# Optimization experiments

Hardware: AMD Instinct MI355X
Metric: run time of the kernel (lower is better)

## Reference

```python
import jax, jax.numpy as jnp
import numpy as np

# Config matching init_kwargs
TAUS = [0.25, 0.5, 0.75]
QWEIGHTS = [0.25, 0.5, 0.25]
T_THRESH = 10
K_DIL = 2
EPS_GIN = 0.0  # (1 + eps) * x term; train_eps=False


def setup_inputs() -> dict:
    key = jax.random.key(0)
    k0, k1, k2, k3 = jax.random.split(key, 4)
    B, N, C, H, CO = 4, 512, 64, 128, 64
    x = jax.random.normal(k0, (B, N, C), dtype=jnp.float32)
    # symmetric random binary adjacency, ~30 avg degree -> dilation active (m > T)
    u = jax.random.uniform(k1, (B, N, N))
    a = (u < 0.03).astype(jnp.float32)
    adj = jnp.maximum(a, jnp.swapaxes(a, 1, 2))
    # last 32 nodes are padding
    mask = jnp.broadcast_to(jnp.arange(N) < (N - 32), (B, N))
    W1 = jax.random.normal(k2, (C, H), dtype=jnp.float32) * (1.0 / np.sqrt(C))
    b1 = jnp.zeros((H,), dtype=jnp.float32)
    W2 = jax.random.normal(k3, (H, CO), dtype=jnp.float32) * (1.0 / np.sqrt(H))
    b2 = jnp.zeros((CO,), dtype=jnp.float32)
    return {"x": x, "adj": adj, "mask": mask, "W1": W1, "b1": b1, "W2": W2, "b2": b2}


def _dilate_adj(adj, mask):
    """Vectorized form of the per-node Python-loop dilation.
    Decisions are based on adj_ (with self-loops), exactly as in the torch loop."""
    B, N, _ = adj.shape
    eye = jnp.eye(N, dtype=bool)
    adj_ = jnp.where(eye[None], 1.0, adj)                 # add self-loops
    nb = (adj_ > 0) & (~eye)[None]                         # neighbors w/o self (B,N,N)
    m = nb.sum(-1)                                         # neighbor count (B,N)
    rank = jnp.cumsum(nb, axis=-1) - 1                     # 0-based position among neighbors
    skip = jnp.where(m > T_THRESH, (m + K_DIL - 1) // K_DIL, 1)  # ceil(m/k); linear mode, layer_idx=1
    do_dil = (skip > 1) & mask                             # masked-out rows are skipped
    removed = nb & do_dil[..., None] & (((rank + 1) % skip[..., None]) == 0)
    rem = removed | jnp.swapaxes(removed, 1, 2)            # symmetric removal
    return jnp.where(rem, 0.0, adj_)


def _weighted_nanquantile_agg(x, valid):
    """Weighted sum of linear-interpolated quantiles over the ragged neighbor dim.
    x: (B,N,C), valid: (B,N,N) bool -> (B,N,C). Empty rows -> 0 (nan_to_num)."""
    B, N, C = x.shape
    big = jnp.finfo(x.dtype).max / 4
    # pool of neighbor features, invalid slots pushed to the end of the sort
    vals = jnp.where(valid[..., None], x[:, None, :, :], big)   # (B,N,N,C)
    sv = jnp.sort(vals, axis=2)
    m = valid.sum(-1)                                           # (B,N)
    mf = m.astype(x.dtype)

    def gather(idx):  # idx (B,N) int -> (B,N,C)
        idxb = jnp.broadcast_to(idx[:, :, None, None], (B, N, 1, C))
        return jnp.take_along_axis(sv, idxb, axis=2)[:, :, 0, :]

    agg = jnp.zeros_like(x)
    for tau, wt in zip(TAUS, QWEIGHTS):
        pos = jnp.clip(tau * (mf - 1.0), 0.0)                   # torch 'linear' interpolation
        lo = jnp.floor(pos).astype(jnp.int32)
        hi = jnp.ceil(pos).astype(jnp.int32)
        frac = (pos - lo.astype(x.dtype))[..., None]
        q = gather(lo) * (1.0 - frac) + gather(hi) * frac
        agg = agg + wt * q
    return jnp.where((m > 0)[..., None], agg, 0.0)


def reference(x, adj, mask, W1, b1, W2, b2):
    dtp = x.dtype
    adj_d = _dilate_adj(adj, mask)
    agg = _weighted_nanquantile_agg(x, adj_d > 0)
    out = (1.0 + EPS_GIN) * x + agg
    h = jax.nn.relu(jnp.einsum('bnc,ch->bnh', out, W1) + b1)    # GIN MLP
    y = jnp.einsum('bnh,ho->bno', h, W2) + b2
    return y * mask[..., None].astype(dtp)
```

## Files before the change

### kernel.cpp

```cpp
#include <hip/hip_runtime.h>
#include <stdint.h>

#define NB 4
#define NN 512
#define NC 64
#define NH 128
#define NCO 64
#define MAXM 64
#define SST 65
#define FBIG 3.0e38f

__device__ inline bool read_mask(const void* mp, int idx) {
    const int* ip = (const int*)mp;
    int w0 = ip[0];
    if (w0 == 1) return ip[idx] != 0;
    if (w0 == 0x3f800000) return ((const float*)mp)[idx] != 0.0f;
    return ((const unsigned char*)mp)[idx] != 0;
}

__global__ __launch_bounds__(256) void prep_kernel(
        const float* __restrict__ adj, const void* __restrict__ maskp,
        const float* __restrict__ W1, const float* __restrict__ W2,
        uint64_t* __restrict__ validbits, float* __restrict__ W1T,
        float* __restrict__ W2T, int dowt)
{
    int wave = (blockIdx.x * 256 + threadIdx.x) >> 6;
    int lane = threadIdx.x & 63;
    if (wave < NB * NN) {
        int i = wave & (NN - 1);
        const float* arow = adj + (size_t)wave * NN;
        uint64_t ball[8];
        int m = 0;
        #pragma unroll
        for (int k = 0; k < 8; ++k) {
            int j = k * 64 + lane;
            bool f = (j != i) && (arow[j] > 0.0f);
            uint64_t bl = __ballot(f);
            ball[k] = bl;
            m += __popcll(bl);
        }
        int skip = (m > 10) ? ((m + 1) >> 1) : 1;
        bool dodil = (skip > 1) && read_mask(maskp, wave);
        int skip2 = skip * 2;
        int prefix = 0;
        #pragma unroll
        for (int k = 0; k < 8; ++k) {
            uint64_t bl = ball[k];
            int rank1 = prefix + __popcll(bl & ((1ull << lane) - 1ull)) + 1;
            bool f = (bl >> lane) & 1ull;
            bool keep = f && !(dodil && (rank1 == skip || rank1 == skip2));
            uint64_t vb = __ballot(keep);
            if (lane == 0) validbits[(size_t)wave * 8 + k] = vb;
            prefix += __popcll(bl);
        }
    }
    if (dowt) {
        int e = blockIdx.x * 256 + threadIdx.x;
        if (e < 8192) {
            int k = e >> 6, c = e & 63;
            W1T[e] = W1[c * NH + k];
        } else if (e < 16384) {
            int e2 = e - 8192;
            int o = e2 >> 7, k = e2 & 127;
            W2T[e2] = W2[k * NCO + o];
        }
    }
}

template<int WIDTH>
__device__ inline float bitonic_sort_lane(float v, int lane) {
    #pragma unroll
    for (int k = 2; k <= WIDTH; k <<= 1) {
        #pragma unroll
        for (int d = k >> 1; d >= 1; d >>= 1) {
            float vp = __shfl_xor(v, d);
            bool keepmin = ((lane & k) == 0) == ((lane & d) == 0);
            v = keepmin ? fminf(v, vp) : fmaxf(v, vp);
        }
    }
    return v;
}

template<bool USE_WT>
__global__ void fused_kernel(
        const float* __restrict__ x,
        const void* __restrict__ maskp,
        const float* __restrict__ W1,
        const float* __restrict__ b1,
        const float* __restrict__ W2,
        const float* __restrict__ b2,
        const uint64_t* __restrict__ validbits,
        const float* __restrict__ W1T,
        const float* __restrict__ W2T,
        float* __restrict__ out)
{
    int row = blockIdx.x;
    int b = row >> 9, i = row & (NN - 1);
    int tid = threadIdx.x, lane = tid & 63, wv = tid >> 6;
    float* outp = out + (size_t)row * NCO;

    if (!read_mask(maskp, row)) {
        if (tid < NCO) outp[tid] = 0.0f;
        return;
    }

    __shared__ float sv[NC * SST];
    __shared__ float s_agg[NC];
    __shared__ __align__(8) uint16_t s_idx[MAXM];
    __shared__ uint64_t s_vb[8];
    __shared__ uint64_t s_vf[8];
    __shared__ int s_cnt;

    float xval = (tid < NC) ? x[(size_t)row * NC + tid] : 0.0f;
    if (tid < 8) s_vb[tid] = validbits[(size_t)row * 8 + tid];
    if (tid < MAXM) s_idx[tid] = (uint16_t)i;
    if (tid == 0) s_cnt = 1;
    __syncthreads();

    int ic = i >> 6;
    uint64_t imask = 1ull << (i & 63);
    #pragma unroll
    for (int it = 0; it < 2; ++it) {
        int j = tid + it * 256;
        bool nb = ((s_vb[j >> 6] >> (j & 63)) & 1ull) &&
                  (validbits[((size_t)(b * NN + j)) * 8 + ic] & imask);
        uint64_t bl = __ballot(nb || (j == i));
        if (lane == 0) s_vf[it * 4 + wv] = bl;
        if (nb) {
            int p = atomicAdd(&s_cnt, 1);
            if (p < MAXM) s_idx[p] = (uint16_t)j;
        }
    }
    __syncthreads();
    int m = s_cnt;

    float mf = (float)m;
    const float taus[3] = {0.25f, 0.5f, 0.75f};
    const float wts[3]  = {0.25f, 0.5f, 0.25f};
    int tlo[3], thi[3];
    float tfrac[3];
    #pragma unroll
    for (int t = 0; t < 3; ++t) {
        float pos = taus[t] * (mf - 1.0f);
        float fl = floorf(pos);
        tlo[t] = (int)fl;
        thi[t] = (int)ceilf(pos);
        tfrac[t] = pos - fl;
    }

    const float* xb = x + (size_t)b * NN * NC;

    if (m <= 32) {
        #pragma unroll
        for (int h = 0; h < 2; ++h) {
            ushort4 id4 = ((const ushort4*)s_idx)[wv * 2 + h];
            int j0 = wv * 8 + h * 4;
            float v0 = xb[(int)id4.x * NC + lane];
            float v1 = xb[(int)id4.y * NC + lane];
            float v2 = xb[(int)id4.z * NC + lane];
            float v3 = xb[(int)id4.w * NC + lane];
            sv[lane * SST + j0 + 0] = (j0 + 0 < m) ? v0 : FBIG;
            sv[lane * SST + j0 + 1] = (j0 + 1 < m) ? v1 : FBIG;
            sv[lane * SST + j0 + 2] = (j0 + 2 < m) ? v2 : FBIG;
            sv[lane * SST + j0 + 3] = (j0 + 3 < m) ? v3 : FBIG;
        }
        __syncthreads();
        int half = lane >> 5, l = lane & 31;
        #pragma unroll
        for (int pp = 0; pp < 8; ++pp) {
            int p = pp * 4 + wv;
            int c = p * 2 + half;
            float v = sv[c * SST + l];
            v = bitonic_sort_lane<32>(v, l);
            float agg = 0.0f;
            #pragma unroll
            for (int t = 0; t < 3; ++t) {
                float vlo = __shfl(v, (half << 5) | tlo[t]);
                float vhi = __shfl(v, (half << 5) | thi[t]);
                agg += wts[t] * (vlo * (1.0f - tfrac[t]) + vhi * tfrac[t]);
            }
            if (l == 0) s_agg[c] = agg;
        }
    } else if (m <= MAXM) {
        #pragma unroll
        for (int h = 0; h < 4; ++h) {
            ushort4 id4 = ((const ushort4*)s_idx)[wv * 4 + h];
            int j0 = wv * 16 + h * 4;
            float v0 = xb[(int)id4.x * NC + lane];
            float v1 = xb[(int)id4.y * NC + lane];
            float v2 = xb[(int)id4.z * NC + lane];
            float v3 = xb[(int)id4.w * NC + lane];
            sv[lane * SST + j0 + 0] = (j0 + 0 < m) ? v0 : FBIG;
            sv[lane * SST + j0 + 1] = (j0 + 1 < m) ? v1 : FBIG;
            sv[lane * SST + j0 + 2] = (j0 + 2 < m) ? v2 : FBIG;
            sv[lane * SST + j0 + 3] = (j0 + 3 < m) ? v3 : FBIG;
        }
        __syncthreads();
        #pragma unroll
        for (int cc = 0; cc < 16; ++cc) {
            int c = cc * 4 + wv;
            float v = sv[c * SST + lane];
            v = bitonic_sort_lane<64>(v, lane);
            float agg = 0.0f;
            #pragma unroll
            for (int t = 0; t < 3; ++t) {
                float vlo = __shfl(v, tlo[t]);
                float vhi = __shfl(v, thi[t]);
                agg += wts[t] * (vlo * (1.0f - tfrac[t]) + vhi * tfrac[t]);
            }
            if (lane == 0) s_agg[c] = agg;
        }
    } else {
        if (tid < NC) {
            int c = tid;
            float qv[6];
            for (int j1 = 0; j1 < NN; ++j1) {
                if (!((s_vf[j1 >> 6] >> (j1 & 63)) & 1ull)) continue;
                float v1 = xb[j1 * NC + c];
                int rs = 0, rl = 0;
                for (int j2 = 0; j2 < NN; ++j2) {
                    if (!((s_vf[j2 >> 6] >> (j2 & 63)) & 1ull)) continue;
                    float v2 = xb[j2 * NC + c];
                    rs += v2 < v1;
                    rl += v2 <= v1;
                }
                #pragma unroll
                for (int t = 0; t < 3; ++t) {
                    if (rs <= tlo[t] && tlo[t] < rl) qv[2 * t]     = v1;
                    if (rs <= thi[t] && thi[t] < rl) qv[2 * t + 1] = v1;
                }
            }
            float agg = 0.0f;
            #pragma unroll
            for (int t = 0; t < 3; ++t)
                agg += wts[t] * (qv[2 * t] * (1.0f - tfrac[t]) + qv[2 * t + 1] * tfrac[t]);
            s_agg[c] = agg;
        }
    }
    __syncthreads();

    float* s_out  = sv;
    float* s_h    = sv + 64;
    float* s_hp   = sv + 256;
    float* s_part = sv + 512;

    if (tid < NC)
        s_out[tid] = xval + s_agg[tid];
    __syncthreads();

    {
        int k = tid & 127, g = tid >> 7;
        float acc = 0.0f;
        if (USE_WT) {
            const float4* w = (const float4*)(W1T + k * 64 + g * 32);
            #pragma unroll
            for (int q = 0; q < 8; ++q) {
                float4 wq = w[q];
                int cc = g * 32 + q * 4;
                acc += wq.x * s_out[cc] + wq.y * s_out[cc + 1]
                     + wq.z * s_out[cc + 2] + wq.w * s_out[cc + 3];
            }
        } else {
            for (int cc = g * 32; cc < g * 32 + 32; ++cc)
                acc += s_out[cc] * W1[cc * NH + k];
        }
        s_hp[g * NH + k] = acc;
    }
    __syncthreads();
    if (tid < NH) {
        float a = s_hp[tid] + s_hp[NH + tid] + b1[tid];
        s_h[tid] = a > 0.0f ? a : 0.0f;
    }
    __syncthreads();

    {
        int o = tid & 63, g = tid >> 6;
        float acc = 0.0f;
        if (USE_WT) {
            const float4* w = (const float4*)(W2T + o * 128 + g * 32);
            #pragma unroll
            for (int q = 0; q < 8; ++q) {
                float4 wq = w[q];
                int k = g * 32 + q * 4;
                acc += wq.x * s_h[k] + wq.y * s_h[k + 1]
                     + wq.z * s_h[k + 2] + wq.w * s_h[k + 3];
            }
        } else {
            for (int k = g * 32; k < g * 32 + 32; ++k)
                acc += s_h[k] * W2[k * NCO + o];
        }
        s_part[g * NCO + o] = acc;
    }
    __syncthreads();
    if (tid < NCO)
        outp[tid] = s_part[tid] + s_part[64 + tid] + s_part[128 + tid]
                  + s_part[192 + tid] + b2[tid];
}

extern "C" void kernel_launch(void* const* d_in, const int* in_sizes, int n_in,
                              void* d_out, int out_size, void* d_ws, size_t ws_size,
                              hipStream_t stream) {
    const float* x   = (const float*)d_in[0];
    const float* adj = (const float*)d_in[1];
    const void* mask = d_in[2];
    const float* W1  = (const float*)d_in[3];
    const float* b1  = (const float*)d_in[4];
    const float* W2  = (const float*)d_in[5];
    const float* b2  = (const float*)d_in[6];
    float* out = (float*)d_out;

    uint64_t* validbits = (uint64_t*)d_ws;
    float* W1T = (float*)((char*)d_ws + 131072);
    float* W2T = W1T + 8192;
    int dowt = (ws_size >= 196608) ? 1 : 0;

    prep_kernel<<<512, 256, 0, stream>>>(adj, mask, W1, W2, validbits, W1T, W2T, dowt);
    if (dowt)
        fused_kernel<true><<<NB * NN, 256, 0, stream>>>(
            x, mask, W1, b1, W2, b2, validbits, W1T, W2T, out);
    else
        fused_kernel<false><<<NB * NN, 256, 0, stream>>>(
            x, mask, W1, b1, W2, b2, validbits, W1T, W2T, out);
}
```

Measured before the change: 115.5 us.

## Sort neighbor features in registers with 4-per-lane bitonic network, drop LDS staging

Replaces the LDS-staged transpose plus one-value-per-lane bitonic sort with a scheme where each lane loads four neighbor values for one channel directly from global memory and sorts them with a hybrid register/shuffle bitonic network. Several channels are handled per wave at once, and quantiles are read back through select plus shuffle. This removes the large shared buffer, a __syncthreads, and many cross-lane shuffle stages, which also shrinks LDS use and may raise occupancy. The cost is uncoalesced gather loads (lanes index different channels and rows) and a more intricate sort network.

```diff
diff --git a/kernel.cpp b/kernel.cpp
--- a/kernel.cpp
+++ b/kernel.cpp
@@ -7,7 +7,6 @@
 #define NH 128
 #define NCO 64
 #define MAXM 64
-#define SST 65
 #define FBIG 3.0e38f
 
 __device__ inline bool read_mask(const void* mp, int idx) {
@@ -67,17 +66,48 @@
     }
 }
 
-template<int WIDTH>
-__device__ inline float bitonic_sort_lane(float v, int lane) {
+__device__ inline void cmpsw(float& a, float& b, bool asc) {
+    float lo = fminf(a, b), hi = fmaxf(a, b);
+    a = asc ? lo : hi;
+    b = asc ? hi : lo;
+}
+__device__ inline void xstage(float q[4], int g, int ld, bool asc) {
     #pragma unroll
-    for (int k = 2; k <= WIDTH; k <<= 1) {
-        #pragma unroll
-        for (int d = k >> 1; d >= 1; d >>= 1) {
-            float vp = __shfl_xor(v, d);
-            bool keepmin = ((lane & k) == 0) == ((lane & d) == 0);
-            v = keepmin ? fminf(v, vp) : fmaxf(v, vp);
-        }
-    }
+    for (int r = 0; r < 4; ++r) {
+        float vp = __shfl_xor(q[r], ld);
+        bool mn = ((g & ld) == 0) == asc;
+        q[r] = mn ? fminf(q[r], vp) : fmaxf(q[r], vp);
+    }
+}
+__device__ inline void regstages(float q[4], bool a) {
+    cmpsw(q[0], q[2], a); cmpsw(q[1], q[3], a);
+    cmpsw(q[0], q[1], a); cmpsw(q[2], q[3], a);
+}
+__device__ inline void sort64_4(float q[4], int g) {
+    cmpsw(q[0], q[1], true);  cmpsw(q[2], q[3], false);
+    regstages(q, (g & 1) == 0);
+    { bool a = (g & 2) == 0; xstage(q, g, 1, a); regstages(q, a); }
+    { bool a = (g & 4) == 0; xstage(q, g, 2, a); xstage(q, g, 1, a);
+      regstages(q, a); }
+    { bool a = (g & 8) == 0; xstage(q, g, 4, a); xstage(q, g, 2, a);
+      xstage(q, g, 1, a); regstages(q, a); }
+    { xstage(q, g, 8, true); xstage(q, g, 4, true); xstage(q, g, 2, true);
+      xstage(q, g, 1, true); regstages(q, true); }
+}
+__device__ inline void sort32_4(float q[4], int g) {
+    cmpsw(q[0], q[1], true);  cmpsw(q[2], q[3], false);
+    regstages(q, (g & 1) == 0);
+    { bool a = (g & 2) == 0; xstage(q, g, 1, a); regstages(q, a); }
+    { bool a = (g & 4) == 0; xstage(q, g, 2, a); xstage(q, g, 1, a);
+      regstages(q, a); }
+    { xstage(q, g, 4, true); xstage(q, g, 2, true); xstage(q, g, 1, true);
+      regstages(q, true); }
+}
+__device__ inline float selreg(const float q[4], int r) {
+    float v = q[0];
+    v = (r == 1) ? q[1] : v;
+    v = (r == 2) ? q[2] : v;
+    v = (r == 3) ? q[3] : v;
     return v;
 }
 
@@ -104,11 +134,14 @@
         return;
     }
 
-    __shared__ float sv[NC * SST];
-    __shared__ float s_agg[NC];
     __shared__ __align__(8) uint16_t s_idx[MAXM];
     __shared__ uint64_t s_vb[8];
     __shared__ uint64_t s_vf[8];
+    __shared__ float s_agg[NC];
+    __shared__ float s_out[NC];
+    __shared__ float s_h[NH];
+    __shared__ float s_hp[2 * NH];
+    __shared__ float s_part[4 * NCO];
     __shared__ int s_cnt;
 
     float xval = (tid < NC) ? x[(size_t)row * NC + tid] : 0.0f;
@@ -151,64 +184,52 @@
     const float* xb = x + (size_t)b * NN * NC;
 
     if (m <= 32) {
+        int g = lane & 7, sg = lane >> 3;
+        ushort4 id4 = ((const ushort4*)s_idx)[g];
+        int j0 = g * 4;
         #pragma unroll
-        for (int h = 0; h < 2; ++h) {
-            ushort4 id4 = ((const ushort4*)s_idx)[wv * 2 + h];
-            int j0 = wv * 8 + h * 4;
-            float v0 = xb[(int)id4.x * NC + lane];
-            float v1 = xb[(int)id4.y * NC + lane];
-            float v2 = xb[(int)id4.z * NC + lane];
-            float v3 = xb[(int)id4.w * NC + lane];
-            sv[lane * SST + j0 + 0] = (j0 + 0 < m) ? v0 : FBIG;
-            sv[lane * SST + j0 + 1] = (j0 + 1 < m) ? v1 : FBIG;
-            sv[lane * SST + j0 + 2] = (j0 + 2 < m) ? v2 : FBIG;
-            sv[lane * SST + j0 + 3] = (j0 + 3 < m) ? v3 : FBIG;
-        }
-        __syncthreads();
-        int half = lane >> 5, l = lane & 31;
+        for (int p = 0; p < 2; ++p) {
+            int c = p * 32 + wv * 8 + sg;
+            float q[4];
+            q[0] = (j0 + 0 < m) ? xb[(int)id4.x * NC + c] : FBIG;
+            q[1] = (j0 + 1 < m) ? xb[(int)id4.y * NC + c] : FBIG;
+            q[2] = (j0 + 2 < m) ? xb[(int)id4.z * NC + c] : FBIG;
+            q[3] = (j0 + 3 < m) ? xb[(int)id4.w * NC + c] : FBIG;
+            sort32_4(q, g);
+            float agg = 0.0f;
+            #pragma unroll
+            for (int t = 0; t < 3; ++t) {
+                float sl = selreg(q, tlo[t] & 3);
+                float vlo = __shfl(sl, (lane & 56) | (tlo[t] >> 2));
+                float sh = selreg(q, thi[t] & 3);
+                float vhi = __shfl(sh, (lane & 56) | (thi[t] >> 2));
+                agg += wts[t] * (vlo * (1.0f - tfrac[t]) + vhi * tfrac[t]);
+            }
+            if (g == 0) s_agg[c] = agg;
+        }
+    } else if (m <= MAXM) {
+        int g = lane & 15, sg = lane >> 4;
+        ushort4 id4 = ((const ushort4*)s_idx)[g];
+        int j0 = g * 4;
         #pragma unroll
-        for (int pp = 0; pp < 8; ++pp) {
-            int p = pp * 4 + wv;
-            int c = p * 2 + half;
-            float v = sv[c * SST + l];
-            v = bitonic_sort_lane<32>(v, l);
+        for (int p = 0; p < 4; ++p) {
+            int c = p * 16 + wv * 4 + sg;
+            float q[4];
+            q[0] = (j0 + 0 < m) ? xb[(int)id4.x * NC + c] : FBIG;
+            q[1] = (j0 + 1 < m) ? xb[(int)id4.y * NC + c] : FBIG;
+            q[2] = (j0 + 2 < m) ? xb[(int)id4.z * NC + c] : FBIG;
+            q[3] = (j0 + 3 < m) ? xb[(int)id4.w * NC + c] : FBIG;
+            sort64_4(q, g);
             float agg = 0.0f;
             #pragma unroll
             for (int t = 0; t < 3; ++t) {
-                float vlo = __shfl(v, (half << 5) | tlo[t]);
-                float vhi = __shfl(v, (half << 5) | thi[t]);
+                float sl = selreg(q, tlo[t] & 3);
+                float vlo = __shfl(sl, (lane & 48) | (tlo[t] >> 2));
+                float sh = selreg(q, thi[t] & 3);
+                float vhi = __shfl(sh, (lane & 48) | (thi[t] >> 2));
                 agg += wts[t] * (vlo * (1.0f - tfrac[t]) + vhi * tfrac[t]);
             }
-            if (l == 0) s_agg[c] = agg;
-        }
-    } else if (m <= MAXM) {
-        #pragma unroll
-        for (int h = 0; h < 4; ++h) {
-            ushort4 id4 = ((const ushort4*)s_idx)[wv * 4 + h];
-            int j0 = wv * 16 + h * 4;
-            float v0 = xb[(int)id4.x * NC + lane];
-            float v1 = xb[(int)id4.y * NC + lane];
-            float v2 = xb[(int)id4.z * NC + lane];
-            float v3 = xb[(int)id4.w * NC + lane];
-            sv[lane * SST + j0 + 0] = (j0 + 0 < m) ? v0 : FBIG;
-            sv[lane * SST + j0 + 1] = (j0 + 1 < m) ? v1 : FBIG;
-            sv[lane * SST + j0 + 2] = (j0 + 2 < m) ? v2 : FBIG;
-            sv[lane * SST + j0 + 3] = (j0 + 3 < m) ? v3 : FBIG;
-        }
-        __syncthreads();
-        #pragma unroll
-        for (int cc = 0; cc < 16; ++cc) {
-            int c = cc * 4 + wv;
-            float v = sv[c * SST + lane];
-            v = bitonic_sort_lane<64>(v, lane);
-            float agg = 0.0f;
-            #pragma unroll
-            for (int t = 0; t < 3; ++t) {
-                float vlo = __shfl(v, tlo[t]);
-                float vhi = __shfl(v, thi[t]);
-                agg += wts[t] * (vlo * (1.0f - tfrac[t]) + vhi * tfrac[t]);
-            }
-            if (lane == 0) s_agg[c] = agg;
+            if (g == 0) s_agg[c] = agg;
         }
     } else {
         if (tid < NC) {
@@ -239,11 +260,6 @@
     }
     __syncthreads();
 
-    float* s_out  = sv;
-    float* s_h    = sv + 64;
-    float* s_hp   = sv + 256;
-    float* s_part = sv + 512;
-
     if (tid < NC)
         s_out[tid] = xval + s_agg[tid];
     __syncthreads();
```

Measured after the change: 126.7 us. 1.1x slower.
